# Kernel tuning notes

Measured on AMD Instinct MI355X. Metric: run time of the kernel, lower is better.

## Reference

```python
import jax, jax.numpy as jnp
import numpy as np


def setup_inputs() -> dict:
    key = jax.random.key(0)
    k_x, k_B, k_C, k_D, k_step = jax.random.split(key, 5)
    Bsz, L, H = 8, 4096, 512
    P = 256  # effective state dim = dim_ssm_state // 2 (conj_sym)
    # s4d_inv init for Lambda (complex, stored as real/imag parts)
    n = jnp.arange(P, dtype=jnp.float32)
    Lambda_re = -0.5 * jnp.ones((P,), dtype=jnp.float32)
    Lambda_im = (P / np.pi) * (P / (2.0 * n + 1.0) - 1.0)
    # lecun_normal-ish init for B (P,H,2) and C (H,P,2), divided by sqrt(2)
    B = jax.random.normal(k_B, (P, H, 2), dtype=jnp.float32) * (1.0 / np.sqrt(H)) / np.sqrt(2.0)
    C = jax.random.normal(k_C, (H, P, 2), dtype=jnp.float32) * (1.0 / np.sqrt(P)) / np.sqrt(2.0)
    D = jax.random.normal(k_D, (H,), dtype=jnp.float32)
    dt_min, dt_max = 1e-3, 1e-1
    log_step = jax.random.uniform(k_step, (P,)) * (np.log(dt_max) - np.log(dt_min)) + np.log(dt_min)
    x = jax.random.normal(k_x, (Bsz, L, H), dtype=jnp.float32)
    return {"x": x, "Lambda_re": Lambda_re, "Lambda_im": Lambda_im,
            "B": B, "C": C, "D": D, "log_step": log_step.astype(jnp.float32)}


def _binary_op(q_i, q_j):
    A_i, b_i = q_i
    A_j, b_j = q_j
    return (A_j * A_i, A_j * b_i + b_j)


def reference(x, Lambda_re, Lambda_im, B, C, D, log_step):
    # Assemble complex params (conj_sym=True)
    Lam = Lambda_re + 1j * Lambda_im          # (P,)
    B_tilde = B[..., 0] + 1j * B[..., 1]      # (P,H)
    C_tilde = C[..., 0] + 1j * C[..., 1]      # (H,P)
    step = jnp.exp(log_step)                  # (P,) step_rescale = 1.0
    # ZOH discretization
    Lambda_bar = jnp.exp(Lam * step)                              # (P,)
    B_bar = ((Lambda_bar - 1.0) / Lam)[:, None] * B_tilde         # (P,H)
    # Bu elements: (Bsz, L, P) complex
    Bu = jnp.einsum('blh,ph->blp', x.astype(B_bar.dtype), B_bar)
    Lam_elems = jnp.broadcast_to(Lambda_bar, Bu.shape)
    # Parallel linear recurrence over time axis
    _, xs = jax.lax.associative_scan(_binary_op, (Lam_elems, Bu), axis=1)
    # Output projection with conjugate symmetry + D skip
    ys = 2.0 * jnp.einsum('blp,hp->blh', xs, C_tilde).real + D * x
    return ys
```

## Files before the change

kernel.cpp:

```cpp
#include <hip/hip_runtime.h>
#include <hip/hip_bf16.h>
#include <hip/hip_fp16.h>
#include <math.h>

#define BSZ 8
#define LSEQ 4096
#define HDIM 512
#define PDIM 256
#define MROWS (BSZ * LSEQ)
#define NDIM 512
#define CHUNK 64
#define NCHUNK (LSEQ / CHUNK)

typedef __attribute__((ext_vector_type(8))) short bf16x8;
typedef __attribute__((ext_vector_type(4))) float f32x4;

__global__ __launch_bounds__(256) void convert_x(const float* __restrict__ x,
                                                 __hip_bfloat16* __restrict__ xb,
                                                 int n4) {
    int i = blockIdx.x * blockDim.x + threadIdx.x;
    if (i >= n4) return;
    float4 v = ((const float4*)x)[i];
    union { ushort4 u; __hip_bfloat16 h[4]; } o;
    o.h[0] = __float2bfloat16(v.x);
    o.h[1] = __float2bfloat16(v.y);
    o.h[2] = __float2bfloat16(v.z);
    o.h[3] = __float2bfloat16(v.w);
    ((ushort4*)xb)[i] = o.u;
}

__global__ void precompute_params(const float* __restrict__ Lre,
                                  const float* __restrict__ Lim,
                                  const float* __restrict__ logstep,
                                  float* __restrict__ f_re, float* __restrict__ f_im,
                                  float* __restrict__ a_re, float* __restrict__ a_im,
                                  float* __restrict__ al_re, float* __restrict__ al_im) {
    int p = threadIdx.x;
    if (p >= PDIM) return;
    double step = exp((double)logstep[p]);
    double dlr = (double)Lre[p], dli = (double)Lim[p];
    double mag = exp(dlr * step);
    double ar = mag * cos(dli * step);
    double ai = mag * sin(dli * step);
    double den = dlr * dlr + dli * dli;
    double nr = ar - 1.0, ni = ai;
    f_re[p] = (float)((nr * dlr + ni * dli) / den);
    f_im[p] = (float)((ni * dlr - nr * dli) / den);
    a_re[p] = (float)ar;
    a_im[p] = (float)ai;
    double cr = ar, ci = ai;
#pragma unroll
    for (int i = 0; i < 6; ++i) {
        double tr = cr * cr - ci * ci;
        double ti = 2.0 * cr * ci;
        cr = tr; ci = ti;
    }
    al_re[p] = (float)cr;
    al_im[p] = (float)ci;
}

__global__ __launch_bounds__(256) void precompute_w1(
    const float* __restrict__ f_re, const float* __restrict__ f_im,
    const float* __restrict__ Bmat,
    __hip_bfloat16* __restrict__ W1T) {
    int idx = blockIdx.x * blockDim.x + threadIdx.x;
    if (idx >= PDIM * HDIM) return;
    int p = idx / HDIM, h = idx % HDIM;
    float fr = f_re[p], fi = f_im[p];
    float br = Bmat[(size_t)(p * HDIM + h) * 2 + 0];
    float bi = Bmat[(size_t)(p * HDIM + h) * 2 + 1];
    W1T[(size_t)(2 * p) * HDIM + h]     = __float2bfloat16(fr * br - fi * bi);
    W1T[(size_t)(2 * p + 1) * HDIM + h] = __float2bfloat16(fr * bi + fi * br);
}

__global__ void precompute_w2(const float* __restrict__ Cmat,
                              __hip_bfloat16* __restrict__ W2T) {
    int idx = blockIdx.x * blockDim.x + threadIdx.x;
    if (idx >= HDIM * PDIM) return;
    int h = idx / PDIM, p = idx % PDIM;
    float cr = Cmat[(size_t)(h * PDIM + p) * 2 + 0];
    float ci = Cmat[(size_t)(h * PDIM + p) * 2 + 1];
    W2T[(size_t)h * NDIM + 2 * p]     = __float2bfloat16(2.0f * cr);
    W2T[(size_t)h * NDIM + 2 * p + 1] = __float2bfloat16(-2.0f * ci);
}

template <typename OT, bool SKIP>
__global__ __launch_bounds__(256) void gemm_bt(
    const __hip_bfloat16* __restrict__ A,
    const __hip_bfloat16* __restrict__ BT,
    OT* __restrict__ C,
    const float* __restrict__ Dvec,
    const __hip_bfloat16* __restrict__ Xskip,
    int M, int N, int K) {
    __shared__ __hip_bfloat16 smA[2 * 128 * 32];
    __shared__ __hip_bfloat16 smB[2 * 128 * 32];

    const int tid = threadIdx.x;
    const int lane = tid & 63;
    const int wave = tid >> 6;
    const int row0 = blockIdx.x * 128;
    const int col0 = blockIdx.y * 128;
    const int wm = (wave >> 1) * 64;
    const int wn = (wave & 1) * 64;

    const int sr = lane >> 2;
    const int sk = (lane & 3) * 8;
    const int quad = lane >> 4;
    const int l15 = lane & 15;

    f32x4 acc[4][4] = {};

    auto stage = [&](int buf, int k0) {
#pragma unroll
        for (int q = 0; q < 2; ++q) {
            const int chunk = wave * 32 + q * 16;
            const __hip_bfloat16* gA = A + (size_t)(row0 + chunk + sr) * K + k0 + sk;
            __builtin_amdgcn_global_load_lds(
                (const __attribute__((address_space(1))) void*)gA,
                (__attribute__((address_space(3))) void*)&smA[buf * 4096 + chunk * 32],
                16, 0, 0);
            const __hip_bfloat16* gB = BT + (size_t)(col0 + chunk + sr) * K + k0 + sk;
            __builtin_amdgcn_global_load_lds(
                (const __attribute__((address_space(1))) void*)gB,
                (__attribute__((address_space(3))) void*)&smB[buf * 4096 + chunk * 32],
                16, 0, 0);
        }
    };

    const int nk = K >> 5;
    stage(0, 0);
    __syncthreads();
    int cur = 0;
    for (int t = 0; t < nk; ++t) {
        if (t + 1 < nk) stage(cur ^ 1, (t + 1) << 5);

        const __hip_bfloat16* sA = &smA[cur * 4096];
        const __hip_bfloat16* sB = &smB[cur * 4096];
        bf16x8 af[4], bfr[4];
#pragma unroll
        for (int i = 0; i < 4; ++i)
            af[i] = *(const bf16x8*)&sA[(wm + i * 16 + l15) * 32 + quad * 8];
#pragma unroll
        for (int j = 0; j < 4; ++j)
            bfr[j] = *(const bf16x8*)&sB[(wn + j * 16 + l15) * 32 + quad * 8];
#pragma unroll
        for (int i = 0; i < 4; ++i)
#pragma unroll
            for (int j = 0; j < 4; ++j)
                acc[i][j] = __builtin_amdgcn_mfma_f32_16x16x32_bf16(
                    af[i], bfr[j], acc[i][j], 0, 0, 0);

        __syncthreads();
        cur ^= 1;
    }

#pragma unroll
    for (int i = 0; i < 4; ++i) {
        const int mbase = row0 + wm + i * 16 + quad * 4;
#pragma unroll
        for (int j = 0; j < 4; ++j) {
            const int col = col0 + wn + j * 16 + l15;
            const float dv = SKIP ? Dvec[col] : 0.0f;
#pragma unroll
            for (int r = 0; r < 4; ++r) {
                const size_t m = (size_t)(mbase + r);
                float v = acc[i][j][r];
                if (SKIP) v += dv * __bfloat162float(Xskip[m * N + col]);
                if constexpr (sizeof(OT) == 2) {
                    C[m * N + col] = OT(v);
                } else {
                    C[m * N + col] = v;
                }
            }
        }
    }
}

__global__ __launch_bounds__(256) void scan_chunks(const __half2* __restrict__ Bu2,
                                                   const float* __restrict__ a_re,
                                                   const float* __restrict__ a_im,
                                                   float2* __restrict__ S) {
    int b = blockIdx.x / NCHUNK;
    int c = blockIdx.x % NCHUNK;
    int p = threadIdx.x;
    float ar = a_re[p], ai = a_im[p];
    float sr = 0.0f, si = 0.0f;
    size_t m0 = (size_t)b * LSEQ + (size_t)c * CHUNK;
    for (int j = 0; j < CHUNK; ++j) {
        float2 u = __half22float2(Bu2[(m0 + j) * PDIM + p]);
        float nsr = ar * sr - ai * si + u.x;
        float nsi = ar * si + ai * sr + u.y;
        sr = nsr; si = nsi;
    }
    S[(size_t)(b * NCHUNK + c) * PDIM + p] = make_float2(sr, si);
}

__global__ __launch_bounds__(256) void scan_carry(const float2* __restrict__ S,
                                                  const float* __restrict__ al_re,
                                                  const float* __restrict__ al_im,
                                                  float2* __restrict__ carry) {
    const int wid = blockIdx.x * 4 + (threadIdx.x >> 6);
    const int b = wid >> 8;
    const int p = wid & 255;
    const int c = threadIdx.x & 63;
    float Ar = al_re[p], Ai = al_im[p];
    float2 s = S[(size_t)(b * NCHUNK + c) * PDIM + p];
    float br = s.x, bi = s.y;
#pragma unroll
    for (int d = 1; d < 64; d <<= 1) {
        float pAr = __shfl_up(Ar, d);
        float pAi = __shfl_up(Ai, d);
        float pbr = __shfl_up(br, d);
        float pbi = __shfl_up(bi, d);
        if (c >= d) {
            float nAr = Ar * pAr - Ai * pAi;
            float nAi = Ar * pAi + Ai * pAr;
            float nbr = Ar * pbr - Ai * pbi + br;
            float nbi = Ar * pbi + Ai * pbr + bi;
            Ar = nAr; Ai = nAi; br = nbr; bi = nbi;
        }
    }
    float er = __shfl_up(br, 1);
    float ei = __shfl_up(bi, 1);
    if (c == 0) { er = 0.0f; ei = 0.0f; }
    carry[(size_t)(b * NCHUNK + c) * PDIM + p] = make_float2(er, ei);
}

__global__ __launch_bounds__(256) void scan_apply(const __half2* __restrict__ Bu2,
                                                  const float* __restrict__ a_re,
                                                  const float* __restrict__ a_im,
                                                  const float2* __restrict__ carry,
                                                  ushort2* __restrict__ xsb2) {
    int b = blockIdx.x / NCHUNK;
    int c = blockIdx.x % NCHUNK;
    int p = threadIdx.x;
    float ar = a_re[p], ai = a_im[p];
    float2 c0 = carry[(size_t)(b * NCHUNK + c) * PDIM + p];
    float sr = c0.x, si = c0.y;
    size_t m0 = (size_t)b * LSEQ + (size_t)c * CHUNK;
    for (int j = 0; j < CHUNK; ++j) {
        size_t idx = (m0 + j) * PDIM + p;
        float2 u = __half22float2(Bu2[idx]);
        float nsr = ar * sr - ai * si + u.x;
        float nsi = ar * si + ai * sr + u.y;
        sr = nsr; si = nsi;
        union { ushort2 u2; __hip_bfloat16 h[2]; } o;
        o.h[0] = __float2bfloat16(sr);
        o.h[1] = __float2bfloat16(si);
        xsb2[idx] = o.u2;
    }
}

extern "C" void kernel_launch(void* const* d_in, const int* in_sizes, int n_in,
                              void* d_out, int out_size, void* d_ws, size_t ws_size,
                              hipStream_t stream) {
    const float* x       = (const float*)d_in[0];
    const float* Lre     = (const float*)d_in[1];
    const float* Lim     = (const float*)d_in[2];
    const float* Bmat    = (const float*)d_in[3];
    const float* Cmat    = (const float*)d_in[4];
    const float* Dvec    = (const float*)d_in[5];
    const float* logstep = (const float*)d_in[6];
    float* out = (float*)d_out;

    char* ws = (char*)d_ws;
    const size_t MB = 1u << 20;
    __hip_bfloat16* xb  = (__hip_bfloat16*)(ws + 0);
    __hip_bfloat16* xsb = (__hip_bfloat16*)(ws + 32 * MB);
    __half* Bu          = (__half*)(ws + 64 * MB);
    __hip_bfloat16* W1T = (__hip_bfloat16*)(ws + 96 * MB);
    __hip_bfloat16* W2T = (__hip_bfloat16*)(ws + 96 * MB + 512 * 1024);
    float*  a_re  = (float*)(ws + 97 * MB);
    float*  a_im  = (float*)(ws + 97 * MB + 4096);
    float*  f_re  = (float*)(ws + 97 * MB + 8192);
    float*  f_im  = (float*)(ws + 97 * MB + 12288);
    float*  al_re = (float*)(ws + 97 * MB + 16384);
    float*  al_im = (float*)(ws + 97 * MB + 20480);
    float2* S     = (float2*)(ws + 98 * MB);
    float2* carry = (float2*)(ws + 99 * MB);

    convert_x<<<(MROWS * HDIM / 4 + 255) / 256, 256, 0, stream>>>(
        x, xb, MROWS * HDIM / 4);
    precompute_params<<<1, 256, 0, stream>>>(Lre, Lim, logstep,
                                             f_re, f_im, a_re, a_im, al_re, al_im);
    precompute_w1<<<(PDIM * HDIM + 255) / 256, 256, 0, stream>>>(
        f_re, f_im, Bmat, W1T);
    precompute_w2<<<(HDIM * PDIM + 255) / 256, 256, 0, stream>>>(Cmat, W2T);

    dim3 ggrid(MROWS / 128, NDIM / 128);
    gemm_bt<__half, false><<<ggrid, 256, 0, stream>>>(
        xb, W1T, Bu, nullptr, nullptr, MROWS, NDIM, HDIM);

    scan_chunks<<<BSZ * NCHUNK, 256, 0, stream>>>((const __half2*)Bu, a_re, a_im, S);
    scan_carry<<<BSZ * PDIM / 4, 256, 0, stream>>>(S, al_re, al_im, carry);
    scan_apply<<<BSZ * NCHUNK, 256, 0, stream>>>((const __half2*)Bu, a_re, a_im,
                                                 carry, (ushort2*)xsb);

    dim3 ggrid2(MROWS / 128, HDIM / 128);
    gemm_bt<float, true><<<ggrid2, 256, 0, stream>>>(
        xsb, W2T, out, Dvec, xb, MROWS, HDIM, NDIM);
}
```

Baseline: 219.7 us.

## Triple-buffer GEMM with swizzled LDS, fuse prep kernels, halve scan chunk size

```diff
diff --git a/kernel.cpp b/kernel.cpp
--- a/kernel.cpp
+++ b/kernel.cpp
@@ -9,25 +9,12 @@
 #define PDIM 256
 #define MROWS (BSZ * LSEQ)
 #define NDIM 512
-#define CHUNK 64
+#define CHUNK 32
 #define NCHUNK (LSEQ / CHUNK)
+#define LOG2CHUNK 5
 
 typedef __attribute__((ext_vector_type(8))) short bf16x8;
 typedef __attribute__((ext_vector_type(4))) float f32x4;
-
-__global__ __launch_bounds__(256) void convert_x(const float* __restrict__ x,
-                                                 __hip_bfloat16* __restrict__ xb,
-                                                 int n4) {
-    int i = blockIdx.x * blockDim.x + threadIdx.x;
-    if (i >= n4) return;
-    float4 v = ((const float4*)x)[i];
-    union { ushort4 u; __hip_bfloat16 h[4]; } o;
-    o.h[0] = __float2bfloat16(v.x);
-    o.h[1] = __float2bfloat16(v.y);
-    o.h[2] = __float2bfloat16(v.z);
-    o.h[3] = __float2bfloat16(v.w);
-    ((ushort4*)xb)[i] = o.u;
-}
 
 __global__ void precompute_params(const float* __restrict__ Lre,
                                   const float* __restrict__ Lim,
@@ -50,7 +37,7 @@
     a_im[p] = (float)ai;
     double cr = ar, ci = ai;
 #pragma unroll
-    for (int i = 0; i < 6; ++i) {
+    for (int i = 0; i < LOG2CHUNK; ++i) {
         double tr = cr * cr - ci * ci;
         double ti = 2.0 * cr * ci;
         cr = tr; ci = ti;
@@ -59,29 +46,39 @@
     al_im[p] = (float)ci;
 }
 
-__global__ __launch_bounds__(256) void precompute_w1(
+#define NCONV (MROWS * HDIM / 4 / 256)
+__global__ __launch_bounds__(256) void prep(
+    const float* __restrict__ x, __hip_bfloat16* __restrict__ xb,
     const float* __restrict__ f_re, const float* __restrict__ f_im,
-    const float* __restrict__ Bmat,
-    __hip_bfloat16* __restrict__ W1T) {
-    int idx = blockIdx.x * blockDim.x + threadIdx.x;
-    if (idx >= PDIM * HDIM) return;
-    int p = idx / HDIM, h = idx % HDIM;
-    float fr = f_re[p], fi = f_im[p];
-    float br = Bmat[(size_t)(p * HDIM + h) * 2 + 0];
-    float bi = Bmat[(size_t)(p * HDIM + h) * 2 + 1];
-    W1T[(size_t)(2 * p) * HDIM + h]     = __float2bfloat16(fr * br - fi * bi);
-    W1T[(size_t)(2 * p + 1) * HDIM + h] = __float2bfloat16(fr * bi + fi * br);
-}
-
-__global__ void precompute_w2(const float* __restrict__ Cmat,
-                              __hip_bfloat16* __restrict__ W2T) {
-    int idx = blockIdx.x * blockDim.x + threadIdx.x;
-    if (idx >= HDIM * PDIM) return;
-    int h = idx / PDIM, p = idx % PDIM;
-    float cr = Cmat[(size_t)(h * PDIM + p) * 2 + 0];
-    float ci = Cmat[(size_t)(h * PDIM + p) * 2 + 1];
-    W2T[(size_t)h * NDIM + 2 * p]     = __float2bfloat16(2.0f * cr);
-    W2T[(size_t)h * NDIM + 2 * p + 1] = __float2bfloat16(-2.0f * ci);
+    const float* __restrict__ Bmat, __hip_bfloat16* __restrict__ W1T,
+    const float* __restrict__ Cmat, __hip_bfloat16* __restrict__ W2T) {
+    const int bid = blockIdx.x;
+    const int tid = threadIdx.x;
+    if (bid < NCONV) {
+        int i = bid * 256 + tid;
+        float4 v = ((const float4*)x)[i];
+        union { ushort4 u; __hip_bfloat16 h[4]; } o;
+        o.h[0] = __float2bfloat16(v.x);
+        o.h[1] = __float2bfloat16(v.y);
+        o.h[2] = __float2bfloat16(v.z);
+        o.h[3] = __float2bfloat16(v.w);
+        ((ushort4*)xb)[i] = o.u;
+    } else if (bid < NCONV + 512) {
+        int idx = (bid - NCONV) * 256 + tid;
+        int p = idx / HDIM, h = idx % HDIM;
+        float fr = f_re[p], fi = f_im[p];
+        float br = Bmat[(size_t)(p * HDIM + h) * 2 + 0];
+        float bi = Bmat[(size_t)(p * HDIM + h) * 2 + 1];
+        W1T[(size_t)(2 * p) * HDIM + h]     = __float2bfloat16(fr * br - fi * bi);
+        W1T[(size_t)(2 * p + 1) * HDIM + h] = __float2bfloat16(fr * bi + fi * br);
+    } else {
+        int idx = (bid - NCONV - 512) * 256 + tid;
+        int h = idx / PDIM, p = idx % PDIM;
+        float cr = Cmat[(size_t)(h * PDIM + p) * 2 + 0];
+        float ci = Cmat[(size_t)(h * PDIM + p) * 2 + 1];
+        W2T[(size_t)h * NDIM + 2 * p]     = __float2bfloat16(2.0f * cr);
+        W2T[(size_t)h * NDIM + 2 * p + 1] = __float2bfloat16(-2.0f * ci);
+    }
 }
 
 template <typename OT, bool SKIP>
@@ -92,8 +89,8 @@
     const float* __restrict__ Dvec,
     const __hip_bfloat16* __restrict__ Xskip,
     int M, int N, int K) {
-    __shared__ __hip_bfloat16 smA[2 * 128 * 32];
-    __shared__ __hip_bfloat16 smB[2 * 128 * 32];
+    __shared__ __hip_bfloat16 smA[3 * 128 * 32];
+    __shared__ __hip_bfloat16 smB[3 * 128 * 32];
 
     const int tid = threadIdx.x;
     const int lane = tid & 63;
@@ -104,13 +101,16 @@
     const int wn = (wave & 1) * 64;
 
     const int sr = lane >> 2;
-    const int sk = (lane & 3) * 8;
+    const int swz_st = ((lane >> 2) & 3) ^ ((lane >> 4) & 3);
+    const int sk = (((lane & 3) ^ swz_st) * 8);
     const int quad = lane >> 4;
     const int l15 = lane & 15;
+    const int rq = ((quad ^ ((l15 & 3) ^ ((l15 >> 2) & 3))) * 8);
 
     f32x4 acc[4][4] = {};
 
-    auto stage = [&](int buf, int k0) {
+    auto stage = [&](int buf, int t) {
+        const int k0 = t << 5;
 #pragma unroll
         for (int q = 0; q < 2; ++q) {
             const int chunk = wave * 32 + q * 16;
@@ -129,20 +129,26 @@
 
     const int nk = K >> 5;
     stage(0, 0);
-    __syncthreads();
+    stage(1, 1);
+    asm volatile("s_waitcnt vmcnt(4)" ::: "memory");
+    __builtin_amdgcn_s_barrier();
+
     int cur = 0;
     for (int t = 0; t < nk; ++t) {
-        if (t + 1 < nk) stage(cur ^ 1, (t + 1) << 5);
+        if (t + 2 < nk) {
+            int st = cur + 2; if (st >= 3) st -= 3;
+            stage(st, t + 2);
+        }
 
         const __hip_bfloat16* sA = &smA[cur * 4096];
         const __hip_bfloat16* sB = &smB[cur * 4096];
         bf16x8 af[4], bfr[4];
 #pragma unroll
         for (int i = 0; i < 4; ++i)
-            af[i] = *(const bf16x8*)&sA[(wm + i * 16 + l15) * 32 + quad * 8];
+            af[i] = *(const bf16x8*)&sA[(wm + i * 16 + l15) * 32 + rq];
 #pragma unroll
         for (int j = 0; j < 4; ++j)
-            bfr[j] = *(const bf16x8*)&sB[(wn + j * 16 + l15) * 32 + quad * 8];
+            bfr[j] = *(const bf16x8*)&sB[(wn + j * 16 + l15) * 32 + rq];
 #pragma unroll
         for (int i = 0; i < 4; ++i)
 #pragma unroll
@@ -150,8 +156,14 @@
                 acc[i][j] = __builtin_amdgcn_mfma_f32_16x16x32_bf16(
                     af[i], bfr[j], acc[i][j], 0, 0, 0);
 
-        __syncthreads();
-        cur ^= 1;
+        if (t + 1 < nk) {
+            if (t + 2 < nk)
+                asm volatile("s_waitcnt vmcnt(4)" ::: "memory");
+            else
+                asm volatile("s_waitcnt vmcnt(0)" ::: "memory");
+            __builtin_amdgcn_s_barrier();
+        }
+        cur += 1; if (cur == 3) cur = 0;
     }
 
 #pragma unroll
@@ -202,17 +214,22 @@
     const int wid = blockIdx.x * 4 + (threadIdx.x >> 6);
     const int b = wid >> 8;
     const int p = wid & 255;
-    const int c = threadIdx.x & 63;
-    float Ar = al_re[p], Ai = al_im[p];
-    float2 s = S[(size_t)(b * NCHUNK + c) * PDIM + p];
-    float br = s.x, bi = s.y;
+    const int lane = threadIdx.x & 63;
+    const int c0 = 2 * lane, c1 = 2 * lane + 1;
+    float alr = al_re[p], ali = al_im[p];
+    float2 s0 = S[(size_t)(b * NCHUNK + c0) * PDIM + p];
+    float2 s1 = S[(size_t)(b * NCHUNK + c1) * PDIM + p];
+    float Ar = alr * alr - ali * ali;
+    float Ai = 2.0f * alr * ali;
+    float br = alr * s0.x - ali * s0.y + s1.x;
+    float bi = alr * s0.y + ali * s0.x + s1.y;
 #pragma unroll
     for (int d = 1; d < 64; d <<= 1) {
         float pAr = __shfl_up(Ar, d);
         float pAi = __shfl_up(Ai, d);
         float pbr = __shfl_up(br, d);
         float pbi = __shfl_up(bi, d);
-        if (c >= d) {
+        if (lane >= d) {
             float nAr = Ar * pAr - Ai * pAi;
             float nAi = Ar * pAi + Ai * pAr;
             float nbr = Ar * pbr - Ai * pbi + br;
@@ -222,8 +239,10 @@
     }
     float er = __shfl_up(br, 1);
     float ei = __shfl_up(bi, 1);
-    if (c == 0) { er = 0.0f; ei = 0.0f; }
-    carry[(size_t)(b * NCHUNK + c) * PDIM + p] = make_float2(er, ei);
+    if (lane == 0) { er = 0.0f; ei = 0.0f; }
+    carry[(size_t)(b * NCHUNK + c0) * PDIM + p] = make_float2(er, ei);
+    carry[(size_t)(b * NCHUNK + c1) * PDIM + p] =
+        make_float2(alr * er - ali * ei + s0.x, alr * ei + ali * er + s0.y);
 }
 
 __global__ __launch_bounds__(256) void scan_apply(const __half2* __restrict__ Bu2,
@@ -277,15 +296,11 @@
     float*  al_re = (float*)(ws + 97 * MB + 16384);
     float*  al_im = (float*)(ws + 97 * MB + 20480);
     float2* S     = (float2*)(ws + 98 * MB);
-    float2* carry = (float2*)(ws + 99 * MB);
-
-    convert_x<<<(MROWS * HDIM / 4 + 255) / 256, 256, 0, stream>>>(
-        x, xb, MROWS * HDIM / 4);
+    float2* carry = (float2*)(ws + 100 * MB);
+
     precompute_params<<<1, 256, 0, stream>>>(Lre, Lim, logstep,
                                              f_re, f_im, a_re, a_im, al_re, al_im);
-    precompute_w1<<<(PDIM * HDIM + 255) / 256, 256, 0, stream>>>(
-        f_re, f_im, Bmat, W1T);
-    precompute_w2<<<(HDIM * PDIM + 255) / 256, 256, 0, stream>>>(Cmat, W2T);
+    prep<<<NCONV + 1024, 256, 0, stream>>>(x, xb, f_re, f_im, Bmat, W1T, Cmat, W2T);
 
     dim3 ggrid(MROWS / 128, NDIM / 128);
     gemm_bt<__half, false><<<ggrid, 256, 0, stream>>>(
```

Result: no change. 217.6 us (-1.0%).
